# Optimization experiments

Hardware: AMD Instinct MI355X
Metric: run time of the kernel (lower is better)

The kernel has to match this reference:

```python
import jax, jax.numpy as jnp
import numpy as np

B, T, N, F = 32, 64, 128, 256
ALPHA, BETA = 1.0, 0.1

def setup_inputs() -> dict:
    key = jax.random.key(0)
    k1, k2 = jax.random.split(key)
    input_tensor = jax.random.normal(k1, (B, T, N, F), dtype=jnp.float32)
    batch_set_size = jax.random.randint(k2, (B, T), 0, N + 1, dtype=jnp.int64)
    return {"input_tensor": input_tensor, "batch_set_size": batch_set_size}

def reference(input_tensor, batch_set_size):
    # Original builds [B,T,N,N] scores = beta*ones + alpha*eye over the :set_size
    # block, then einsum 'btnn,btnf->btnf' extracts only the DIAGONAL:
    #   diag[b,t,n] = alpha + beta  if n < set_size[b,t] else 0
    # So the math is a ragged mask times a scalar scale (dropout is identity in eval).
    n_idx = jnp.arange(input_tensor.shape[2])                     # [N]
    mask = (n_idx[None, None, :] < batch_set_size[:, :, None])    # [B,T,N] bool
    scale = jnp.asarray(ALPHA + BETA, dtype=input_tensor.dtype)
    return input_tensor * (mask[..., None].astype(input_tensor.dtype) * scale)
```

## Files before the change

kernel.cpp:

```cpp
#include <hip/hip_runtime.h>
#include <hip/hip_bf16.h>


typedef float vfloat4 __attribute__((ext_vector_type(4)));

#define N_DIM 128
#define F_DIM 256
#define ROW_F4 (F_DIM / 4)
#define BT_F4 (N_DIM * ROW_F4)
#define BLOCK 256
#define SCALE 1.1f

__global__ __launch_bounds__(BLOCK) void mask_scale_kernel(
    const vfloat4* __restrict__ in,
    const int* __restrict__ sizes,
    vfloat4* __restrict__ out) {
    const int bt = blockIdx.x;
    const int set = sizes[bt];
    const long long base = (long long)bt * BT_F4;
    const int split = set * ROW_F4;

    const vfloat4* in_b = in + base;
    vfloat4* out_b = out + base;

#pragma unroll 4
    for (int j = threadIdx.x; j < split; j += BLOCK) {
        vfloat4 v = __builtin_nontemporal_load(&in_b[j]);
        v *= SCALE;
        __builtin_nontemporal_store(v, &out_b[j]);
    }

    const vfloat4 z = (vfloat4)(0.f);
#pragma unroll 4
    for (int j = split + (int)threadIdx.x; j < BT_F4; j += BLOCK) {
        __builtin_nontemporal_store(z, &out_b[j]);
    }
}

extern "C" void kernel_launch(void* const* d_in, const int* in_sizes, int n_in,
                              void* d_out, int out_size, void* d_ws, size_t ws_size,
                              hipStream_t stream) {
    const vfloat4* in = (const vfloat4*)d_in[0];
    const int* sizes = (const int*)d_in[1];
    vfloat4* out = (vfloat4*)d_out;

    const int bt_count = in_sizes[1];
    mask_scale_kernel<<<bt_count, BLOCK, 0, stream>>>(in, sizes, out);
}
```

Baseline: 409.4 us.

## Replace per-(b,t) blocks with flat grid-stride loop over all elements

Each block no longer owns one (b,t) slice. The kernel now uses a fixed 2048-block grid-stride loop over the whole flattened tensor, and every element looks up its own set size and masks itself. This evens out work across blocks, since the ragged set sizes made the old per-slice blocks unbalanced. The cost is an extra sizes lookup per element, and the total size is now hardcoded into the kernel.

```diff
diff --git a/kernel.cpp b/kernel.cpp
--- a/kernel.cpp
+++ b/kernel.cpp
@@ -4,36 +4,28 @@
 
 typedef float vfloat4 __attribute__((ext_vector_type(4)));
 
-#define N_DIM 128
-#define F_DIM 256
-#define ROW_F4 (F_DIM / 4)
-#define BT_F4 (N_DIM * ROW_F4)
+#define TOTAL_F4 (32 * 64 * 128 * 64)
 #define BLOCK 256
+#define GRID 2048
 #define SCALE 1.1f
 
 __global__ __launch_bounds__(BLOCK) void mask_scale_kernel(
     const vfloat4* __restrict__ in,
     const int* __restrict__ sizes,
     vfloat4* __restrict__ out) {
-    const int bt = blockIdx.x;
-    const int set = sizes[bt];
-    const long long base = (long long)bt * BT_F4;
-    const int split = set * ROW_F4;
-
-    const vfloat4* in_b = in + base;
-    vfloat4* out_b = out + base;
+    const int tid = blockIdx.x * BLOCK + threadIdx.x;
+    const int stride = GRID * BLOCK;
 
 #pragma unroll 4
-    for (int j = threadIdx.x; j < split; j += BLOCK) {
-        vfloat4 v = __builtin_nontemporal_load(&in_b[j]);
-        v *= SCALE;
-        __builtin_nontemporal_store(v, &out_b[j]);
-    }
-
-    const vfloat4 z = (vfloat4)(0.f);
-#pragma unroll 4
-    for (int j = split + (int)threadIdx.x; j < BT_F4; j += BLOCK) {
-        __builtin_nontemporal_store(z, &out_b[j]);
+    for (int j = tid; j < TOTAL_F4; j += stride) {
+        const int bt = j >> 13;
+        const int n = (j >> 6) & 127;
+        vfloat4 v = (vfloat4)(0.f);
+        if (n < sizes[bt]) {
+            v = __builtin_nontemporal_load(&in[j]);
+            v *= SCALE;
+        }
+        __builtin_nontemporal_store(v, &out[j]);
     }
 }
 
@@ -44,6 +36,5 @@
     const int* sizes = (const int*)d_in[1];
     vfloat4* out = (vfloat4*)d_out;
 
-    const int bt_count = in_sizes[1];
-    mask_scale_kernel<<<bt_count, BLOCK, 0, stream>>>(in, sizes, out);
+    mask_scale_kernel<<<GRID, BLOCK, 0, stream>>>(in, sizes, out);
 }
```

Measured after the change: 410.2 us. No clear change (+0.2%).
